# Optimization experiments

Measured on AMD Instinct MI355X. Metric: run time of the kernel, lower is better.

## Reference

```python
import jax, jax.numpy as jnp
import numpy as np

B, N, D, U = 8, 2048, 512, 512

def setup_inputs() -> dict:
    key = jax.random.key(0)
    ks = jax.random.split(key, 7)
    s = 1.0 / np.sqrt(D)
    return {
        "inputs": jax.random.normal(ks[0], (B, N, D), dtype=jnp.float32),
        "Wq": jax.random.normal(ks[1], (D, U), dtype=jnp.float32) * s,
        "bq": jnp.zeros((U,), dtype=jnp.float32),
        "Wk": jax.random.normal(ks[2], (D, U), dtype=jnp.float32) * s,
        "bk": jnp.zeros((U,), dtype=jnp.float32),
        "Wv": jax.random.normal(ks[3], (D, U), dtype=jnp.float32) * s,
        "bv": jnp.zeros((U,), dtype=jnp.float32),
    }

def reference(inputs, Wq, bq, Wk, bk, Wv, bv):
    # Dense projections (Keras Dense: x @ W + b)
    Q = inputs @ Wq + bq  # [B, N, U]
    K = inputs @ Wk + bk  # [B, N, U]
    V = inputs @ Wv + bv  # [B, N, U]
    # NOTE: original module has NO 1/sqrt(d) scaling
    scores = jnp.einsum("bnu,bmu->bnm", Q, K)  # [B, N, N]
    attn = jax.nn.softmax(scores, axis=-1)
    return jnp.einsum("bnm,bmu->bnu", attn, V)  # [B, N, U]
```

## Files before the change

kernel.cpp:

```cpp
#include <hip/hip_runtime.h>


typedef _Float16 f16;
typedef _Float16 f16x4 __attribute__((ext_vector_type(4)));
typedef _Float16 f16x8 __attribute__((ext_vector_type(8)));
typedef float f32x4 __attribute__((ext_vector_type(4)));
typedef short s16x8 __attribute__((ext_vector_type(8)));
typedef unsigned short u16;

#define OFS 96.0f

__device__ __forceinline__ void stage16(const void* g, void* lds_uniform) {
    __builtin_amdgcn_global_load_lds(
        (const __attribute__((address_space(1))) void*)g,
        (__attribute__((address_space(3))) void*)lds_uniform,
        16, 0, 0);
}

__device__ __forceinline__ u16 f2bf(float f) {
    unsigned u = __builtin_bit_cast(unsigned, f);
    u = (u + 0x7FFF + ((u >> 16) & 1)) >> 16;
    return (u16)u;
}
__device__ __forceinline__ float bf2f(u16 b) {
    return __builtin_bit_cast(float, (unsigned)b << 16);
}

__global__ __launch_bounds__(256) void prep_fused(
    const float* __restrict__ X,
    const float* __restrict__ Wq, const float* __restrict__ Wk,
    const float* __restrict__ Wv,
    const float* __restrict__ bq, const float* __restrict__ bk,
    const float* __restrict__ bv,
    f16* __restrict__ X16, f16* __restrict__ Wt, float* __restrict__ biases,
    float* __restrict__ rowsum) {
    __shared__ float t[32][33];
    const int bid = blockIdx.x, tid = threadIdx.x;
    if (bid < 8192) {
        int i = (bid * 256 + tid) * 4;
        float4 v = *(const float4*)(X + i);
        f16x4 o;
        o[0] = (f16)v.x; o[1] = (f16)v.y; o[2] = (f16)v.z; o[3] = (f16)v.w;
        *(f16x4*)(X16 + i) = o;
    } else if (bid < 8960) {
        int id = bid - 8192;
        int z = id >> 8, rem = id & 255;
        int u0 = (rem & 15) * 32, d0 = (rem >> 4) * 32;
        const float* W = (z == 0) ? Wq : (z == 1 ? Wk : Wv);
        f16* outp = Wt + (size_t)z * 262144;
        int tx = tid & 31, ty = tid >> 5;
#pragma unroll
        for (int r = 0; r < 4; r++)
            t[ty + 8 * r][tx] = W[(size_t)(d0 + ty + 8 * r) * 512 + u0 + tx];
        __syncthreads();
#pragma unroll
        for (int r = 0; r < 4; r++)
            outp[(size_t)(u0 + ty + 8 * r) * 512 + d0 + tx] = (f16)t[tx][ty + 8 * r];
    } else if (bid == 8960) {
#pragma unroll
        for (int j = 0; j < 6; j++) {
            int i = j * 256 + tid;
            float v = (i < 512) ? bq[i] : (i < 1024) ? bk[i - 512] : bv[i - 1024];
            biases[i] = v;
        }
    } else {
        int id = bid - 8961;
        float4 z4 = {0.f, 0.f, 0.f, 0.f};
        ((float4*)rowsum)[id * 256 + tid] = z4;
    }
}

template <int MODE>
__device__ __forceinline__ void gemm_core(
    const u16* __restrict__ A, int lda,
    const u16* __restrict__ Bt, int ldb,
    int m0, int n0, int K,
    const float* __restrict__ bias, float* __restrict__ rs,
    void* __restrict__ Cv, int ldc,
    u16* As, u16* Bs) {
    __shared__ float rowbuf[128];

    const int tid = threadIdx.x;
    const int wid = tid >> 6, lane = tid & 63;

    if (MODE == 2) {
        if (tid < 128) rowbuf[tid] = bias[m0 + tid];
    }

    const int schunk = (lane & 7) ^ ((lane >> 3) & 7);
    const u16* gA = A + (size_t)(m0 + wid * 32 + (lane >> 3)) * lda + schunk * 8;
    const u16* gB = Bt + (size_t)(n0 + wid * 32 + (lane >> 3)) * ldb + schunk * 8;
    u16* ldsA = As + (wid * 32) * 64;
    u16* ldsB = Bs + (wid * 32) * 64;

    const int wr = wid >> 1, wc = wid & 1;
    const int frow = lane & 15;
    const int f7 = frow & 7;
    const int c_lo = (lane >> 4) ^ f7;
    const int c_hi = ((lane >> 4) | 4) ^ f7;
    const u16* fA_lo = As + (wr * 64 + frow) * 64 + c_lo * 8;
    const u16* fA_hi = As + (wr * 64 + frow) * 64 + c_hi * 8;
    const u16* fB_lo = Bs + (wc * 64 + frow) * 64 + c_lo * 8;
    const u16* fB_hi = Bs + (wc * 64 + frow) * 64 + c_hi * 8;

    f32x4 acc[4][4] = {};

    for (int kt = 0; kt < K; kt += 64) {
#pragma unroll
        for (int j = 0; j < 4; j++)
            stage16(gA + (size_t)(j * 8) * lda, ldsA + (j * 8) * 64);
#pragma unroll
        for (int j = 0; j < 4; j++)
            stage16(gB + (size_t)(j * 8) * ldb, ldsB + (j * 8) * 64);
        gA += 64; gB += 64;
        __syncthreads();

#pragma unroll
        for (int half = 0; half < 2; half++) {
            const u16* pA = half ? fA_hi : fA_lo;
            const u16* pB = half ? fB_hi : fB_lo;
            f16x8 af[4], bf[4];
#pragma unroll
            for (int i = 0; i < 4; i++) af[i] = *(const f16x8*)(const f16*)(pA + i * 16 * 64);
#pragma unroll
            for (int i = 0; i < 4; i++) bf[i] = *(const f16x8*)(const f16*)(pB + i * 16 * 64);
#pragma unroll
            for (int mi = 0; mi < 4; mi++)
#pragma unroll
                for (int ni = 0; ni < 4; ni++)
                    acc[mi][ni] = __builtin_amdgcn_mfma_f32_16x16x32_f16(
                        af[mi], bf[ni], acc[mi][ni], 0, 0, 0);
        }
        __syncthreads();
    }

    const int crow0 = m0 + wr * 64 + ((lane >> 4) << 2);
    const int ccol0 = n0 + wc * 64 + (lane & 15);

    if (MODE == 1) {
        f16* C = (f16*)Cv;
#pragma unroll
        for (int mi = 0; mi < 4; mi++)
#pragma unroll
            for (int ni = 0; ni < 4; ni++) {
                float cb = bias[ccol0 + ni * 16];
#pragma unroll
                for (int r = 0; r < 4; r++)
                    C[(size_t)(crow0 + mi * 16 + r) * ldc + ccol0 + ni * 16] =
                        (f16)(acc[mi][ni][r] + cb);
            }
    } else if (MODE == 2) {
        u16* C = (u16*)Cv;
#pragma unroll
        for (int mi = 0; mi < 4; mi++)
#pragma unroll
            for (int ni = 0; ni < 4; ni++)
#pragma unroll
                for (int r = 0; r < 4; r++) {
                    float rb = rowbuf[crow0 + mi * 16 + r - m0];
                    C[(size_t)(crow0 + mi * 16 + r) * ldc + ccol0 + ni * 16] =
                        f2bf(acc[mi][ni][r] + rb);
                }
    } else {
        u16* C = (u16*)Cv;
#pragma unroll
        for (int mi = 0; mi < 4; mi++)
#pragma unroll
            for (int r = 0; r < 4; r++) {
                float rsum = 0.0f;
#pragma unroll
                for (int ni = 0; ni < 4; ni++) {
                    u16 b = f2bf(__expf(acc[mi][ni][r] - OFS));
                    C[(size_t)(crow0 + mi * 16 + r) * ldc + ccol0 + ni * 16] = b;
                    rsum += bf2f(b);
                }
#pragma unroll
                for (int o = 1; o < 16; o <<= 1)
                    rsum += __shfl_xor(rsum, o, 64);
                if ((lane & 15) == 0)
                    atomicAdd(rs + crow0 + mi * 16 + r, rsum);
            }
    }
}

__global__ __launch_bounds__(256) void proj_fused(
    const u16* __restrict__ X16, const u16* __restrict__ Wt,
    const float* __restrict__ biases,
    u16* __restrict__ QK, u16* __restrict__ Vt) {
    __shared__ __align__(16) u16 As[128 * 64];
    __shared__ __align__(16) u16 Bs[128 * 64];
    const int bid = blockIdx.x;
    if (bid < 1024) {
        int z = bid >> 9, rem = bid & 511;
        int bx = rem & 127, by = rem >> 7;
        gemm_core<1>(X16, 512, Wt + (size_t)z * 262144, 512,
                     bx * 128, by * 128, 512,
                     biases + z * 512, nullptr,
                     QK + (size_t)z * 8388608, 512, As, Bs);
    } else {
        int id = bid - 1024;
        int bz = id & 7, rem = id >> 3;
        int bx = rem & 3, by = rem >> 2;
        gemm_core<2>(Wt + (size_t)2 * 262144, 512,
                     X16 + (size_t)bz * 1048576, 512,
                     bx * 128, by * 128, 512,
                     biases + 1024, nullptr,
                     Vt + (size_t)bz * 1048576, 2048, As, Bs);
    }
}

__global__ __launch_bounds__(256) void score_gemm(
    const u16* __restrict__ Q, const u16* __restrict__ Kk,
    u16* __restrict__ P, float* __restrict__ rowsum) {
    __shared__ __align__(16) u16 As[128 * 64];
    __shared__ __align__(16) u16 Bs[128 * 64];
    const int i = blockIdx.x;
    const int z = i & 7, y = (i >> 3) & 15, x = i >> 7;
    gemm_core<3>(Q + (size_t)z * 1048576, 512,
                 Kk + (size_t)z * 1048576, 512,
                 x * 128, y * 128, 512,
                 nullptr, rowsum + z * 2048,
                 P + (size_t)z * 4194304, 2048, As, Bs);
}

__global__ __launch_bounds__(256) void pv_gemm(
    const u16* __restrict__ Pg, const u16* __restrict__ Vtg,
    float* __restrict__ rowsum, float* __restrict__ outg) {
    __shared__ __align__(16) u16 As[64 * 64];
    __shared__ __align__(16) u16 Bs[128 * 64];
    __shared__ float rowbuf[64];

    const int i = blockIdx.x;
    const int z = i & 7, y = (i >> 3) & 3, x = i >> 5;
    const int m0 = x * 64, n0 = y * 128;
    const u16* A = Pg + (size_t)z * 4194304;
    const u16* Bt = Vtg + (size_t)z * 1048576;
    float* C = outg + (size_t)z * 1048576;
    const float* rs = rowsum + z * 2048;

    const int tid = threadIdx.x;
    const int w = tid >> 6, lane = tid & 63;

    if (tid < 64) rowbuf[tid] = rs[m0 + tid];

    const int schunk = (lane & 7) ^ ((lane >> 3) & 7);
    const u16* gA = A + (size_t)(m0 + w * 16 + (lane >> 3)) * 2048 + schunk * 8;
    u16* ldsA = As + (w * 16) * 64;
    const u16* gB = Bt + (size_t)(n0 + w * 32 + (lane >> 3)) * 2048 + schunk * 8;
    u16* ldsB = Bs + (w * 32) * 64;

    const int frow = lane & 15;
    const int f7 = frow & 7;
    const int c_lo = (lane >> 4) ^ f7;
    const int c_hi = ((lane >> 4) | 4) ^ f7;
    const u16* fA_lo = As + frow * 64 + c_lo * 8;
    const u16* fA_hi = As + frow * 64 + c_hi * 8;
    const u16* fB_lo = Bs + (w * 32 + frow) * 64 + c_lo * 8;
    const u16* fB_hi = Bs + (w * 32 + frow) * 64 + c_hi * 8;

    f32x4 acc[4][2] = {};

    for (int kt = 0; kt < 2048; kt += 64) {
#pragma unroll
        for (int j = 0; j < 2; j++)
            stage16(gA + (size_t)(j * 8) * 2048, ldsA + (j * 8) * 64);
#pragma unroll
        for (int j = 0; j < 4; j++)
            stage16(gB + (size_t)(j * 8) * 2048, ldsB + (j * 8) * 64);
        gA += 64; gB += 64;
        __syncthreads();

#pragma unroll
        for (int half = 0; half < 2; half++) {
            const u16* pA = half ? fA_hi : fA_lo;
            const u16* pB = half ? fB_hi : fB_lo;
            s16x8 af[4], bf[2];
#pragma unroll
            for (int mi = 0; mi < 4; mi++) af[mi] = *(const s16x8*)(pA + mi * 16 * 64);
#pragma unroll
            for (int ni = 0; ni < 2; ni++) bf[ni] = *(const s16x8*)(pB + ni * 16 * 64);
#pragma unroll
            for (int mi = 0; mi < 4; mi++)
#pragma unroll
                for (int ni = 0; ni < 2; ni++)
                    acc[mi][ni] = __builtin_amdgcn_mfma_f32_16x16x32_bf16(
                        af[mi], bf[ni], acc[mi][ni], 0, 0, 0);
        }
        __syncthreads();
    }

    const int crow0 = m0 + ((lane >> 4) << 2);
    const int ccol0 = n0 + w * 32 + (lane & 15);
#pragma unroll
    for (int mi = 0; mi < 4; mi++) {
        float inv[4];
#pragma unroll
        for (int r = 0; r < 4; r++)
            inv[r] = 1.0f / rowbuf[((lane >> 4) << 2) + mi * 16 + r];
#pragma unroll
        for (int ni = 0; ni < 2; ni++)
#pragma unroll
            for (int r = 0; r < 4; r++)
                C[(size_t)(crow0 + mi * 16 + r) * 512 + ccol0 + ni * 16] =
                    acc[mi][ni][r] * inv[r];
    }
}


extern "C" void kernel_launch(void* const* d_in, const int* in_sizes, int n_in,
                              void* d_out, int out_size, void* d_ws, size_t ws_size,
                              hipStream_t stream) {
    const float* X  = (const float*)d_in[0];
    const float* Wq = (const float*)d_in[1];
    const float* bq = (const float*)d_in[2];
    const float* Wk = (const float*)d_in[3];
    const float* bk = (const float*)d_in[4];
    const float* Wv = (const float*)d_in[5];
    const float* bv = (const float*)d_in[6];
    float* out = (float*)d_out;
    char* ws = (char*)d_ws;

    f16*   X16    = (f16*)ws;
    f16*   Wt     = (f16*)(ws + 16777216);
    float* biases = (float*)(ws + 18350080);
    u16*   QK     = (u16*)(ws + 18356224);
    u16*   Vt     = (u16*)(ws + 51910656);
    u16*   P      = (u16*)(ws + 68687872);
    float* rowsum = (float*)(ws + 135796736);

    prep_fused<<<8977, 256, 0, stream>>>(X, Wq, Wk, Wv, bq, bk, bv,
                                         X16, Wt, biases, rowsum);

    proj_fused<<<1536, 256, 0, stream>>>((const u16*)X16, (const u16*)Wt,
                                         biases, QK, Vt);

    score_gemm<<<2048, 256, 0, stream>>>(QK, QK + (size_t)8388608, P, rowsum);

    pv_gemm<<<1024, 256, 0, stream>>>(P, Vt, rowsum, out);
}
```

Baseline: 222.0 us.

## Fuse score and PV GEMMs into one kernel with per-band completion counters

Merges the score GEMM and the PV GEMM into a single launch of 1024 blocks. Each block first computes two score tiles, then bumps an atomic counter for that tile's batch and row band. It then spin-waits until all 16 column tiles of the band it needs are done before running its PV tile. This is meant to remove the kernel boundary and let PV work overlap the tail of score work. It relies on all 1024 blocks being co-resident (launch bounds of 4 blocks per CU) to avoid deadlock, and it adds fences and spin-wait overhead.

```diff
diff --git a/kernel.cpp b/kernel.cpp
--- a/kernel.cpp
+++ b/kernel.cpp
@@ -33,7 +33,7 @@
     const float* __restrict__ bq, const float* __restrict__ bk,
     const float* __restrict__ bv,
     f16* __restrict__ X16, f16* __restrict__ Wt, float* __restrict__ biases,
-    float* __restrict__ rowsum) {
+    float* __restrict__ rowsum, int* __restrict__ cnt) {
     __shared__ float t[32][33];
     const int bid = blockIdx.x, tid = threadIdx.x;
     if (bid < 8192) {
@@ -63,10 +63,12 @@
             float v = (i < 512) ? bq[i] : (i < 1024) ? bk[i - 512] : bv[i - 1024];
             biases[i] = v;
         }
-    } else {
+    } else if (bid < 8977) {
         int id = bid - 8961;
         float4 z4 = {0.f, 0.f, 0.f, 0.f};
         ((float4*)rowsum)[id * 256 + tid] = z4;
+    } else {
+        if (tid < 128) cnt[tid] = 0;
     }
 }
 
@@ -209,39 +211,50 @@
     }
 }
 
-__global__ __launch_bounds__(256) void score_gemm(
+__global__ __launch_bounds__(256, 4) void attn_fused(
     const u16* __restrict__ Q, const u16* __restrict__ Kk,
-    u16* __restrict__ P, float* __restrict__ rowsum) {
+    u16* __restrict__ P, float* __restrict__ rowsum, int* __restrict__ cnt,
+    const u16* __restrict__ Vtg, float* __restrict__ outg) {
     __shared__ __align__(16) u16 As[128 * 64];
     __shared__ __align__(16) u16 Bs[128 * 64];
-    const int i = blockIdx.x;
-    const int z = i & 7, y = (i >> 3) & 15, x = i >> 7;
-    gemm_core<3>(Q + (size_t)z * 1048576, 512,
-                 Kk + (size_t)z * 1048576, 512,
-                 x * 128, y * 128, 512,
-                 nullptr, rowsum + z * 2048,
-                 P + (size_t)z * 4194304, 2048, As, Bs);
-}
-
-__global__ __launch_bounds__(256) void pv_gemm(
-    const u16* __restrict__ Pg, const u16* __restrict__ Vtg,
-    float* __restrict__ rowsum, float* __restrict__ outg) {
-    __shared__ __align__(16) u16 As[64 * 64];
-    __shared__ __align__(16) u16 Bs[128 * 64];
-    __shared__ float rowbuf[64];
-
-    const int i = blockIdx.x;
-    const int z = i & 7, y = (i >> 3) & 3, x = i >> 5;
-    const int m0 = x * 64, n0 = y * 128;
-    const u16* A = Pg + (size_t)z * 4194304;
+    __shared__ float prow[64];
+
+    const int bid = blockIdx.x;
+    const int tid = threadIdx.x;
+
+#pragma unroll 1
+    for (int u = 0; u < 2; u++) {
+        int i = bid + u * 1024;
+        int z = i & 7, y = (i >> 3) & 15, x = i >> 7;
+        gemm_core<3>(Q + (size_t)z * 1048576, 512,
+                     Kk + (size_t)z * 1048576, 512,
+                     x * 128, y * 128, 512,
+                     nullptr, rowsum + z * 2048,
+                     P + (size_t)z * 4194304, 2048, As, Bs);
+        __threadfence();
+        __syncthreads();
+        if (tid == 0) atomicAdd(&cnt[z * 16 + x], 1);
+    }
+
+    const int z = bid & 7, yy = (bid >> 3) & 3, x = bid >> 5;
+    const int m0 = x * 64, n0 = yy * 128;
+    const int band = x >> 1;
+
+    if (tid == 0) {
+        while (__hip_atomic_load(&cnt[z * 16 + band], __ATOMIC_ACQUIRE,
+                                 __HIP_MEMORY_SCOPE_AGENT) < 16)
+            __builtin_amdgcn_s_sleep(8);
+    }
+    __syncthreads();
+    __threadfence();
+
+    const u16* A = P + (size_t)z * 4194304;
     const u16* Bt = Vtg + (size_t)z * 1048576;
     float* C = outg + (size_t)z * 1048576;
     const float* rs = rowsum + z * 2048;
 
-    const int tid = threadIdx.x;
     const int w = tid >> 6, lane = tid & 63;
-
-    if (tid < 64) rowbuf[tid] = rs[m0 + tid];
+    if (tid < 64) prow[tid] = rs[m0 + tid];
 
     const int schunk = (lane & 7) ^ ((lane >> 3) & 7);
     const u16* gA = A + (size_t)(m0 + w * 16 + (lane >> 3)) * 2048 + schunk * 8;
@@ -296,7 +309,7 @@
         float inv[4];
 #pragma unroll
         for (int r = 0; r < 4; r++)
-            inv[r] = 1.0f / rowbuf[((lane >> 4) << 2) + mi * 16 + r];
+            inv[r] = 1.0f / prow[((lane >> 4) << 2) + mi * 16 + r];
 #pragma unroll
         for (int ni = 0; ni < 2; ni++)
 #pragma unroll
@@ -327,14 +340,14 @@
     u16*   Vt     = (u16*)(ws + 51910656);
     u16*   P      = (u16*)(ws + 68687872);
     float* rowsum = (float*)(ws + 135796736);
-
-    prep_fused<<<8977, 256, 0, stream>>>(X, Wq, Wk, Wv, bq, bk, bv,
-                                         X16, Wt, biases, rowsum);
+    int*   cnt    = (int*)(ws + 135862272);
+
+    prep_fused<<<8978, 256, 0, stream>>>(X, Wq, Wk, Wv, bq, bk, bv,
+                                         X16, Wt, biases, rowsum, cnt);
 
     proj_fused<<<1536, 256, 0, stream>>>((const u16*)X16, (const u16*)Wt,
                                          biases, QK, Vt);
 
-    score_gemm<<<2048, 256, 0, stream>>>(QK, QK + (size_t)8388608, P, rowsum);
-
-    pv_gemm<<<1024, 256, 0, stream>>>(P, Vt, rowsum, out);
-}
+    attn_fused<<<1024, 256, 0, stream>>>(QK, QK + (size_t)8388608,
+                                         P, rowsum, cnt, Vt, out);
+}
```

New measurement: 726.6 us. 3.27x slower.
